# Performance work log

Measured on AMD Instinct MI355X. Metric: run time of the kernel, lower is better.

Reference implementation:

```python
import jax, jax.numpy as jnp
import numpy as np

D_HEAD = 64  # module's self.heads scaling constant


def setup_inputs() -> dict:
    key = jax.random.key(0)
    kq, kk, kv = jax.random.split(key, 3)
    N, HW, C = 4, 4096, 64
    Q = jax.random.normal(kq, (N, HW, C), dtype=jnp.float32)
    K = jax.random.normal(kk, (N, HW, C), dtype=jnp.float32)
    V = jax.random.normal(kv, (N, HW, C), dtype=jnp.float32)
    return {"Q": Q, "K": K, "V": V}


def reference(Q, K, V):
    # logits[n, q, k] = Q[n,q,:] . K[n,k,:] / sqrt(d_head)
    scale = 1.0 / jnp.sqrt(jnp.asarray(D_HEAD, dtype=Q.dtype))
    logits = jnp.einsum("nqc,nkc->nqk", Q, K) * scale  # [N, HW, HW]
    # NOTE: softmax over the QUERY axis (dim=1), non-standard
    attn = jax.nn.softmax(logits, axis=1)
    return jnp.einsum("nqk,nkc->nqc", attn, V)
```

## Files before the change

kernel.cpp:

```cpp
#include <hip/hip_runtime.h>

#define NB 4
#define HWN 4096
#define CD 64
#define NSTRIDE (HWN * CD)

typedef short short8 __attribute__((ext_vector_type(8), may_alias));
typedef float f32x4 __attribute__((ext_vector_type(4), may_alias));

__device__ constexpr float C1 = 0.18033688011112042f;

__device__ __forceinline__ unsigned short f2bf(float f) {
    unsigned u = __builtin_bit_cast(unsigned, f);
    u = (u + 0x7FFFu + ((u >> 16) & 1u)) >> 16;
    return (unsigned short)u;
}

__device__ __forceinline__ float fexp2(float x) {
#if __has_builtin(__builtin_amdgcn_exp2f)
    return __builtin_amdgcn_exp2f(x);
#else
    return exp2f(x);
#endif
}

__device__ __forceinline__ size_t qk_swz(int row, int c) {
    return (size_t)(row >> 4) * 1024 + (c >> 5) * 512 +
           ((((c >> 3) & 3) * 16 + (row & 15)) * 8) + (c & 7);
}

__global__ __launch_bounds__(256) void cvt_qk(const float* __restrict__ Q,
                                              const float* __restrict__ K,
                                              unsigned short* __restrict__ Qs,
                                              unsigned short* __restrict__ Ks) {
    int i = (blockIdx.x * 256 + threadIdx.x) * 4;
    int rg = i >> 6, c = i & 63;
    int n = rg >> 12, r = rg & 4095;
    float4 q = *(const float4*)(Q + i);
    float4 k = *(const float4*)(K + i);
    ushort4 qo, ko;
    qo.x = f2bf(q.x); qo.y = f2bf(q.y); qo.z = f2bf(q.z); qo.w = f2bf(q.w);
    ko.x = f2bf(k.x); ko.y = f2bf(k.y); ko.z = f2bf(k.z); ko.w = f2bf(k.w);
    size_t off = (size_t)n * NSTRIDE + qk_swz(r, c);
    *(ushort4*)(Qs + off) = qo;
    *(ushort4*)(Ks + off) = ko;
}

__global__ __launch_bounds__(256, 4) void lsum_kernel(const unsigned short* __restrict__ Qs,
                                                      const unsigned short* __restrict__ Ks,
                                                      float* __restrict__ l) {
    int tid = threadIdx.x;
    int w = tid >> 6, lane = tid & 63, quad = lane >> 4, m16 = lane & 15;
    int n = blockIdx.y;
    int kbase = blockIdx.x * 128 + w * 32;

    const unsigned short* Kp = Ks + (size_t)n * NSTRIDE + (kbase >> 4) * 1024 + lane * 8;
    short8 ka0 = *(const short8*)(Kp);
    short8 ka1 = *(const short8*)(Kp + 512);
    short8 kb0 = *(const short8*)(Kp + 1024);
    short8 kb1 = *(const short8*)(Kp + 1536);

    const unsigned short* Qp = Qs + (size_t)n * NSTRIDE + blockIdx.z * 32768 + lane * 8;

    float lA[4] = {0.f, 0.f, 0.f, 0.f};
    float lB[4] = {0.f, 0.f, 0.f, 0.f};
#pragma unroll 4
    for (int qc = 0; qc < 32; ++qc) {
        short8 qf0 = *(const short8*)(Qp);
        short8 qf1 = *(const short8*)(Qp + 512);
        f32x4 a = {0.f, 0.f, 0.f, 0.f}, b = {0.f, 0.f, 0.f, 0.f};
        a = __builtin_amdgcn_mfma_f32_16x16x32_bf16(ka0, qf0, a, 0, 0, 0);
        a = __builtin_amdgcn_mfma_f32_16x16x32_bf16(ka1, qf1, a, 0, 0, 0);
        b = __builtin_amdgcn_mfma_f32_16x16x32_bf16(kb0, qf0, b, 0, 0, 0);
        b = __builtin_amdgcn_mfma_f32_16x16x32_bf16(kb1, qf1, b, 0, 0, 0);
#pragma unroll
        for (int r = 0; r < 4; ++r) {
            lA[r] += fexp2(a[r] * C1);
            lB[r] += fexp2(b[r] * C1);
        }
        Qp += 1024;
    }
#pragma unroll
    for (int r = 0; r < 4; ++r)
        for (int d = 1; d < 16; d <<= 1) {
            lA[r] += __shfl_xor(lA[r], d);
            lB[r] += __shfl_xor(lB[r], d);
        }
    if (m16 == 0) {
        float* lp = l + n * HWN + kbase + quad * 4;
#pragma unroll
        for (int r = 0; r < 4; ++r) {
            atomicAdd(lp + r, lA[r]);
            atomicAdd(lp + 16 + r, lB[r]);
        }
    }
}

__global__ __launch_bounds__(256) void prep_v(const float* __restrict__ V,
                                              const float* __restrict__ l,
                                              unsigned short* __restrict__ Vts) {
    __shared__ float rl[64];
    __shared__ float tile[64][65];
    int tid = threadIdx.x, n = blockIdx.y, kbase = blockIdx.x * 64;
    if (tid < 64) rl[tid] = 1.0f / l[n * HWN + kbase + tid];
    __syncthreads();
#pragma unroll
    for (int i = 0; i < 16; ++i) {
        int e = i * 256 + tid;
        int k = e >> 6, c = e & 63;
        tile[c][k] = V[((size_t)(n * HWN + kbase + k)) * CD + c] * rl[k];
    }
    __syncthreads();
#pragma unroll
    for (int i = 0; i < 2; ++i) {
        int s = i * 256 + tid;
        int c = s >> 3, kg = s & 7;
        int kl = kg * 8;
        int kgl = kbase + kl;
        short8 v;
#pragma unroll
        for (int j = 0; j < 8; ++j) v[j] = (short)f2bf(tile[c][kl + j]);
        size_t off = (size_t)n * NSTRIDE + (size_t)(kgl >> 5) * 2048 + (c >> 4) * 512 +
                     ((((kgl >> 3) & 3) * 16 + (c & 15)) * 8);
        *(short8*)(Vts + off) = v;
    }
}

__global__ __launch_bounds__(256, 4) void attn_kernel(const unsigned short* __restrict__ Qs,
                                                      const unsigned short* __restrict__ Ks,
                                                      const unsigned short* __restrict__ Vts,
                                                      float* __restrict__ partial,
                                                      int nseg) {
    __shared__ short plds[4][16][40];
    int tid = threadIdx.x;
    int w = tid >> 6, lane = tid & 63, quad = lane >> 4, m16 = lane & 15;
    int n = blockIdx.y;
    int qbase = blockIdx.x * 64 + w * 16;

    const unsigned short* Qp = Qs + (size_t)n * NSTRIDE + (qbase >> 4) * 1024 + lane * 8;
    short8 qf0 = *(const short8*)(Qp);
    short8 qf1 = *(const short8*)(Qp + 512);

    size_t kofs = (size_t)blockIdx.z * (size_t)nseg * 8 * 2048;
    const unsigned short* Kp = Ks + (size_t)n * NSTRIDE + kofs + lane * 8;
    const unsigned short* Vp = Vts + (size_t)n * NSTRIDE + kofs + lane * 8;

    f32x4 o[4];
#pragma unroll
    for (int ct = 0; ct < 4; ++ct) o[ct] = f32x4{0.f, 0.f, 0.f, 0.f};

    short* pw = &plds[w][0][0];

    for (int seg = 0; seg < nseg; ++seg) {
#pragma unroll
        for (int it = 0; it < 8; ++it) {
            short8 kf00 = *(const short8*)(Kp);
            short8 kf01 = *(const short8*)(Kp + 512);
            short8 kf10 = *(const short8*)(Kp + 1024);
            short8 kf11 = *(const short8*)(Kp + 1536);
            f32x4 s0 = {0.f, 0.f, 0.f, 0.f}, s1 = {0.f, 0.f, 0.f, 0.f};
            s0 = __builtin_amdgcn_mfma_f32_16x16x32_bf16(qf0, kf00, s0, 0, 0, 0);
            s0 = __builtin_amdgcn_mfma_f32_16x16x32_bf16(qf1, kf01, s0, 0, 0, 0);
            s1 = __builtin_amdgcn_mfma_f32_16x16x32_bf16(qf0, kf10, s1, 0, 0, 0);
            s1 = __builtin_amdgcn_mfma_f32_16x16x32_bf16(qf1, kf11, s1, 0, 0, 0);

            short* prow = pw + (quad * 4) * 40 + m16;
#pragma unroll
            for (int r = 0; r < 4; ++r) {
                prow[r * 40]      = (short)f2bf(fexp2(s0[r] * C1));
                prow[r * 40 + 16] = (short)f2bf(fexp2(s1[r] * C1));
            }
            short8 pf = *(const short8*)(pw + m16 * 40 + quad * 8);

#pragma unroll
            for (int ct = 0; ct < 4; ++ct) {
                short8 vf = *(const short8*)(Vp + ct * 512);
                o[ct] = __builtin_amdgcn_mfma_f32_16x16x32_bf16(pf, vf, o[ct], 0, 0, 0);
            }
            Kp += 2048;
            Vp += 2048;
        }
        __syncthreads();
    }

    float* pp = partial + (size_t)blockIdx.z * (NB * HWN * CD) +
                ((size_t)(n * HWN + qbase + quad * 4)) * CD + m16;
#pragma unroll
    for (int ct = 0; ct < 4; ++ct)
#pragma unroll
        for (int r = 0; r < 4; ++r)
            pp[r * CD + ct * 16] = o[ct][r];
}

__global__ __launch_bounds__(256) void reduce_out(const float* __restrict__ p,
                                                  float* __restrict__ out, int ns) {
    int i = (blockIdx.x * 256 + threadIdx.x) * 4;
    f32x4 a = *(const f32x4*)(p + i);
    for (int s = 1; s < ns; ++s)
        a = a + *(const f32x4*)(p + (size_t)s * (NB * HWN * CD) + i);
    *(f32x4*)(out + i) = a;
}

extern "C" void kernel_launch(void* const* d_in, const int* in_sizes, int n_in,
                              void* d_out, int out_size, void* d_ws, size_t ws_size,
                              hipStream_t stream) {
    const float* Q = (const float*)d_in[0];
    const float* K = (const float*)d_in[1];
    const float* V = (const float*)d_in[2];
    float* out = (float*)d_out;

    char* ws = (char*)d_ws;
    unsigned short* Qs  = (unsigned short*)(ws);
    unsigned short* Ks  = (unsigned short*)(ws + (1u << 21));
    unsigned short* Vts = (unsigned short*)(ws + (2u << 21));
    float* l       = (float*)(ws + (3u << 21));
    float* partial = (float*)(ws + (4u << 21));

    size_t base = (size_t)(4u << 21);
    size_t slice = (size_t)NB * HWN * CD * sizeof(float);
    int ns = (ws_size >= base + 4 * slice) ? 4 : 2;
    int nseg = (HWN / ns) / 32 / 8;

    hipMemsetAsync(l, 0, (size_t)NB * HWN * sizeof(float), stream);

    cvt_qk<<<1024, 256, 0, stream>>>(Q, K, Qs, Ks);
    lsum_kernel<<<dim3(32, NB, 8), 256, 0, stream>>>(Qs, Ks, l);
    prep_v<<<dim3(64, NB), 256, 0, stream>>>(V, l, Vts);
    attn_kernel<<<dim3(64, NB, ns), 256, 0, stream>>>(Qs, Ks, Vts, partial, nseg);
    reduce_out<<<1024, 256, 0, stream>>>(partial, out, ns);
}
```

Measured before the change: 133.0 us.

## Software-pipeline attention loop with double-buffered P tile and prefetched K/V

The attention kernel's inner loop is restructured into a software pipeline. It prefetches the next K and V fragments into registers and double-buffers the per-wave P tile in LDS, so the exp/P write for one step overlaps the PV MFMAs of the previous step. The per-segment __syncthreads is removed. The lsum kernel is split across twice as many z-blocks with a register prefetch of Q and an occupancy hint of 8, which raises parallelism and latency hiding. These changes add register pressure and rely on per-wave LDS ordering with no block barrier.

```diff
diff --git a/kernel.cpp b/kernel.cpp
--- a/kernel.cpp
+++ b/kernel.cpp
@@ -46,7 +46,7 @@
     *(ushort4*)(Ks + off) = ko;
 }
 
-__global__ __launch_bounds__(256, 4) void lsum_kernel(const unsigned short* __restrict__ Qs,
+__global__ __launch_bounds__(256, 8) void lsum_kernel(const unsigned short* __restrict__ Qs,
                                                       const unsigned short* __restrict__ Ks,
                                                       float* __restrict__ l) {
     int tid = threadIdx.x;
@@ -60,24 +60,29 @@
     short8 kb0 = *(const short8*)(Kp + 1024);
     short8 kb1 = *(const short8*)(Kp + 1536);
 
-    const unsigned short* Qp = Qs + (size_t)n * NSTRIDE + blockIdx.z * 32768 + lane * 8;
+    const unsigned short* Qp = Qs + (size_t)n * NSTRIDE + blockIdx.z * 16384 + lane * 8;
+
+    short8 qc0 = *(const short8*)(Qp);
+    short8 qc1 = *(const short8*)(Qp + 512);
+    Qp += 1024;
 
     float lA[4] = {0.f, 0.f, 0.f, 0.f};
     float lB[4] = {0.f, 0.f, 0.f, 0.f};
-#pragma unroll 4
-    for (int qc = 0; qc < 32; ++qc) {
-        short8 qf0 = *(const short8*)(Qp);
-        short8 qf1 = *(const short8*)(Qp + 512);
+#pragma unroll 2
+    for (int qc = 0; qc < 16; ++qc) {
+        short8 qn0 = *(const short8*)(Qp);
+        short8 qn1 = *(const short8*)(Qp + 512);
         f32x4 a = {0.f, 0.f, 0.f, 0.f}, b = {0.f, 0.f, 0.f, 0.f};
-        a = __builtin_amdgcn_mfma_f32_16x16x32_bf16(ka0, qf0, a, 0, 0, 0);
-        a = __builtin_amdgcn_mfma_f32_16x16x32_bf16(ka1, qf1, a, 0, 0, 0);
-        b = __builtin_amdgcn_mfma_f32_16x16x32_bf16(kb0, qf0, b, 0, 0, 0);
-        b = __builtin_amdgcn_mfma_f32_16x16x32_bf16(kb1, qf1, b, 0, 0, 0);
+        a = __builtin_amdgcn_mfma_f32_16x16x32_bf16(ka0, qc0, a, 0, 0, 0);
+        a = __builtin_amdgcn_mfma_f32_16x16x32_bf16(ka1, qc1, a, 0, 0, 0);
+        b = __builtin_amdgcn_mfma_f32_16x16x32_bf16(kb0, qc0, b, 0, 0, 0);
+        b = __builtin_amdgcn_mfma_f32_16x16x32_bf16(kb1, qc1, b, 0, 0, 0);
 #pragma unroll
         for (int r = 0; r < 4; ++r) {
             lA[r] += fexp2(a[r] * C1);
             lB[r] += fexp2(b[r] * C1);
         }
+        qc0 = qn0; qc1 = qn1;
         Qp += 1024;
     }
 #pragma unroll
@@ -130,8 +135,8 @@
                                                       const unsigned short* __restrict__ Ks,
                                                       const unsigned short* __restrict__ Vts,
                                                       float* __restrict__ partial,
-                                                      int nseg) {
-    __shared__ short plds[4][16][40];
+                                                      int nit) {
+    __shared__ short plds[4][2][16][40];
     int tid = threadIdx.x;
     int w = tid >> 6, lane = tid & 63, quad = lane >> 4, m16 = lane & 15;
     int n = blockIdx.y;
@@ -141,7 +146,7 @@
     short8 qf0 = *(const short8*)(Qp);
     short8 qf1 = *(const short8*)(Qp + 512);
 
-    size_t kofs = (size_t)blockIdx.z * (size_t)nseg * 8 * 2048;
+    size_t kofs = (size_t)blockIdx.z * (size_t)nit * 2048;
     const unsigned short* Kp = Ks + (size_t)n * NSTRIDE + kofs + lane * 8;
     const unsigned short* Vp = Vts + (size_t)n * NSTRIDE + kofs + lane * 8;
 
@@ -149,38 +154,89 @@
 #pragma unroll
     for (int ct = 0; ct < 4; ++ct) o[ct] = f32x4{0.f, 0.f, 0.f, 0.f};
 
-    short* pw = &plds[w][0][0];
-
-    for (int seg = 0; seg < nseg; ++seg) {
-#pragma unroll
-        for (int it = 0; it < 8; ++it) {
-            short8 kf00 = *(const short8*)(Kp);
-            short8 kf01 = *(const short8*)(Kp + 512);
-            short8 kf10 = *(const short8*)(Kp + 1024);
-            short8 kf11 = *(const short8*)(Kp + 1536);
-            f32x4 s0 = {0.f, 0.f, 0.f, 0.f}, s1 = {0.f, 0.f, 0.f, 0.f};
-            s0 = __builtin_amdgcn_mfma_f32_16x16x32_bf16(qf0, kf00, s0, 0, 0, 0);
-            s0 = __builtin_amdgcn_mfma_f32_16x16x32_bf16(qf1, kf01, s0, 0, 0, 0);
-            s1 = __builtin_amdgcn_mfma_f32_16x16x32_bf16(qf0, kf10, s1, 0, 0, 0);
-            s1 = __builtin_amdgcn_mfma_f32_16x16x32_bf16(qf1, kf11, s1, 0, 0, 0);
-
-            short* prow = pw + (quad * 4) * 40 + m16;
-#pragma unroll
-            for (int r = 0; r < 4; ++r) {
-                prow[r * 40]      = (short)f2bf(fexp2(s0[r] * C1));
-                prow[r * 40 + 16] = (short)f2bf(fexp2(s1[r] * C1));
-            }
-            short8 pf = *(const short8*)(pw + m16 * 40 + quad * 8);
-
-#pragma unroll
-            for (int ct = 0; ct < 4; ++ct) {
-                short8 vf = *(const short8*)(Vp + ct * 512);
-                o[ct] = __builtin_amdgcn_mfma_f32_16x16x32_bf16(pf, vf, o[ct], 0, 0, 0);
-            }
-            Kp += 2048;
-            Vp += 2048;
-        }
-        __syncthreads();
+    short* pw0 = &plds[w][0][0][0];
+    short* pw1 = &plds[w][1][0][0];
+    int wr_off = (quad * 4) * 40 + m16;
+    int rd_off = m16 * 40 + quad * 8;
+
+    short8 kc0, kc1, kc2, kc3, vp0, vp1, vp2, vp3;
+
+    kc0 = *(const short8*)(Kp);
+    kc1 = *(const short8*)(Kp + 512);
+    kc2 = *(const short8*)(Kp + 1024);
+    kc3 = *(const short8*)(Kp + 1536);
+    Kp += 2048;
+    vp0 = *(const short8*)(Vp);
+    vp1 = *(const short8*)(Vp + 512);
+    vp2 = *(const short8*)(Vp + 1024);
+    vp3 = *(const short8*)(Vp + 1536);
+    Vp += 2048;
+    {
+        f32x4 s0 = {0.f, 0.f, 0.f, 0.f}, s1 = {0.f, 0.f, 0.f, 0.f};
+        s0 = __builtin_amdgcn_mfma_f32_16x16x32_bf16(qf0, kc0, s0, 0, 0, 0);
+        s0 = __builtin_amdgcn_mfma_f32_16x16x32_bf16(qf1, kc1, s0, 0, 0, 0);
+        s1 = __builtin_amdgcn_mfma_f32_16x16x32_bf16(qf0, kc2, s1, 0, 0, 0);
+        s1 = __builtin_amdgcn_mfma_f32_16x16x32_bf16(qf1, kc3, s1, 0, 0, 0);
+        short* prow = pw0 + wr_off;
+#pragma unroll
+        for (int r = 0; r < 4; ++r) {
+            prow[r * 40]      = (short)f2bf(fexp2(s0[r] * C1));
+            prow[r * 40 + 16] = (short)f2bf(fexp2(s1[r] * C1));
+        }
+    }
+    kc0 = *(const short8*)(Kp);
+    kc1 = *(const short8*)(Kp + 512);
+    kc2 = *(const short8*)(Kp + 1024);
+    kc3 = *(const short8*)(Kp + 1536);
+    Kp += 2048;
+
+#pragma unroll 2
+    for (int it = 1; it < nit; ++it) {
+        short8 kn0 = *(const short8*)(Kp);
+        short8 kn1 = *(const short8*)(Kp + 512);
+        short8 kn2 = *(const short8*)(Kp + 1024);
+        short8 kn3 = *(const short8*)(Kp + 1536);
+        Kp += 2048;
+        short8 vn0 = *(const short8*)(Vp);
+        short8 vn1 = *(const short8*)(Vp + 512);
+        short8 vn2 = *(const short8*)(Vp + 1024);
+        short8 vn3 = *(const short8*)(Vp + 1536);
+        Vp += 2048;
+
+        f32x4 s0 = {0.f, 0.f, 0.f, 0.f}, s1 = {0.f, 0.f, 0.f, 0.f};
+        s0 = __builtin_amdgcn_mfma_f32_16x16x32_bf16(qf0, kc0, s0, 0, 0, 0);
+        s0 = __builtin_amdgcn_mfma_f32_16x16x32_bf16(qf1, kc1, s0, 0, 0, 0);
+        s1 = __builtin_amdgcn_mfma_f32_16x16x32_bf16(qf0, kc2, s1, 0, 0, 0);
+        s1 = __builtin_amdgcn_mfma_f32_16x16x32_bf16(qf1, kc3, s1, 0, 0, 0);
+
+        short* pr = ((it & 1) ? pw0 : pw1) + rd_off;
+        short8 pf = *(const short8*)pr;
+#pragma unroll
+        for (int ct = 0; ct < 4; ++ct) {
+            short8 vf;
+            switch (ct) { case 0: vf = vp0; break; case 1: vf = vp1; break;
+                          case 2: vf = vp2; break; default: vf = vp3; }
+            o[ct] = __builtin_amdgcn_mfma_f32_16x16x32_bf16(pf, vf, o[ct], 0, 0, 0);
+        }
+
+        short* prow = ((it & 1) ? pw1 : pw0) + wr_off;
+#pragma unroll
+        for (int r = 0; r < 4; ++r) {
+            prow[r * 40]      = (short)f2bf(fexp2(s0[r] * C1));
+            prow[r * 40 + 16] = (short)f2bf(fexp2(s1[r] * C1));
+        }
+
+        kc0 = kn0; kc1 = kn1; kc2 = kn2; kc3 = kn3;
+        vp0 = vn0; vp1 = vn1; vp2 = vn2; vp3 = vn3;
+    }
+
+    {
+        short* pr = ((nit & 1) ? pw0 : pw1) + rd_off;
+        short8 pf = *(const short8*)pr;
+        o[0] = __builtin_amdgcn_mfma_f32_16x16x32_bf16(pf, vp0, o[0], 0, 0, 0);
+        o[1] = __builtin_amdgcn_mfma_f32_16x16x32_bf16(pf, vp1, o[1], 0, 0, 0);
+        o[2] = __builtin_amdgcn_mfma_f32_16x16x32_bf16(pf, vp2, o[2], 0, 0, 0);
+        o[3] = __builtin_amdgcn_mfma_f32_16x16x32_bf16(pf, vp3, o[3], 0, 0, 0);
     }
 
     float* pp = partial + (size_t)blockIdx.z * (NB * HWN * CD) +
@@ -219,13 +275,13 @@
     size_t base = (size_t)(4u << 21);
     size_t slice = (size_t)NB * HWN * CD * sizeof(float);
     int ns = (ws_size >= base + 4 * slice) ? 4 : 2;
-    int nseg = (HWN / ns) / 32 / 8;
+    int nit = HWN / ns / 32;
 
     hipMemsetAsync(l, 0, (size_t)NB * HWN * sizeof(float), stream);
 
     cvt_qk<<<1024, 256, 0, stream>>>(Q, K, Qs, Ks);
-    lsum_kernel<<<dim3(32, NB, 8), 256, 0, stream>>>(Qs, Ks, l);
+    lsum_kernel<<<dim3(32, NB, 16), 256, 0, stream>>>(Qs, Ks, l);
     prep_v<<<dim3(64, NB), 256, 0, stream>>>(V, l, Vts);
-    attn_kernel<<<dim3(64, NB, ns), 256, 0, stream>>>(Qs, Ks, Vts, partial, nseg);
+    attn_kernel<<<dim3(64, NB, ns), 256, 0, stream>>>(Qs, Ks, Vts, partial, nit);
     reduce_out<<<1024, 256, 0, stream>>>(partial, out, ns);
 }
```

Result: faster. 124.3 us (-6.5%).

## Stage K/V and Q tiles through LDS with async double-buffered loads

Applied to the files above, without the earlier changes.

The attention kernel now copies K and V tiles into double-buffered shared memory using global_load_lds. Each wave handles 32 queries instead of 16, so each K/V fragment is reused twice. The PV matmul is software-pipelined one iteration behind the QK exp stage, and the key-axis split grows to 8 segments when the workspace allows. The lsum kernel also stages Q through LDS, raises its occupancy target and uses twice as many z-blocks. The aim is to cut redundant global loads and hide load latency, at the cost of more LDS, extra barriers per iteration and larger partial buffers to reduce.

```diff
diff --git a/kernel.cpp b/kernel.cpp
--- a/kernel.cpp
+++ b/kernel.cpp
@@ -22,6 +22,12 @@
 #else
     return exp2f(x);
 #endif
+}
+
+__device__ __forceinline__ void gload_lds16(const unsigned short* g, unsigned short* lds) {
+    __builtin_amdgcn_global_load_lds(
+        (const __attribute__((address_space(1))) unsigned int*)g,
+        (__attribute__((address_space(3))) unsigned int*)lds, 16, 0, 0);
 }
 
 __device__ __forceinline__ size_t qk_swz(int row, int c) {
@@ -46,9 +52,10 @@
     *(ushort4*)(Ks + off) = ko;
 }
 
-__global__ __launch_bounds__(256, 4) void lsum_kernel(const unsigned short* __restrict__ Qs,
+__global__ __launch_bounds__(256, 8) void lsum_kernel(const unsigned short* __restrict__ Qs,
                                                       const unsigned short* __restrict__ Ks,
                                                       float* __restrict__ l) {
+    __shared__ unsigned short qstage[2][1024];
     int tid = threadIdx.x;
     int w = tid >> 6, lane = tid & 63, quad = lane >> 4, m16 = lane & 15;
     int n = blockIdx.y;
@@ -60,14 +67,19 @@
     short8 kb0 = *(const short8*)(Kp + 1024);
     short8 kb1 = *(const short8*)(Kp + 1536);
 
-    const unsigned short* Qp = Qs + (size_t)n * NSTRIDE + blockIdx.z * 32768 + lane * 8;
+    const unsigned short* Qsrc = Qs + (size_t)n * NSTRIDE + blockIdx.z * 16384;
+
+    if (w < 2) gload_lds16(Qsrc + w * 512 + lane * 8, &qstage[0][w * 512]);
 
     float lA[4] = {0.f, 0.f, 0.f, 0.f};
     float lB[4] = {0.f, 0.f, 0.f, 0.f};
-#pragma unroll 4
-    for (int qc = 0; qc < 32; ++qc) {
-        short8 qf0 = *(const short8*)(Qp);
-        short8 qf1 = *(const short8*)(Qp + 512);
+    for (int it = 0; it < 16; ++it) {
+        __syncthreads();
+        if (it + 1 < 16 && w < 2)
+            gload_lds16(Qsrc + (it + 1) * 1024 + w * 512 + lane * 8,
+                        &qstage[(it + 1) & 1][w * 512]);
+        short8 qf0 = *(const short8*)&qstage[it & 1][lane * 8];
+        short8 qf1 = *(const short8*)&qstage[it & 1][512 + lane * 8];
         f32x4 a = {0.f, 0.f, 0.f, 0.f}, b = {0.f, 0.f, 0.f, 0.f};
         a = __builtin_amdgcn_mfma_f32_16x16x32_bf16(ka0, qf0, a, 0, 0, 0);
         a = __builtin_amdgcn_mfma_f32_16x16x32_bf16(ka1, qf1, a, 0, 0, 0);
@@ -78,7 +90,6 @@
             lA[r] += fexp2(a[r] * C1);
             lB[r] += fexp2(b[r] * C1);
         }
-        Qp += 1024;
     }
 #pragma unroll
     for (int r = 0; r < 4; ++r)
@@ -130,57 +141,107 @@
                                                       const unsigned short* __restrict__ Ks,
                                                       const unsigned short* __restrict__ Vts,
                                                       float* __restrict__ partial,
-                                                      int nseg) {
-    __shared__ short plds[4][16][40];
+                                                      int nit) {
+    __shared__ unsigned short stage[2][4096];
+    __shared__ short plds[4][2][2][16][40];
     int tid = threadIdx.x;
     int w = tid >> 6, lane = tid & 63, quad = lane >> 4, m16 = lane & 15;
     int n = blockIdx.y;
-    int qbase = blockIdx.x * 64 + w * 16;
+    int qbase = blockIdx.x * 128 + w * 32;
 
     const unsigned short* Qp = Qs + (size_t)n * NSTRIDE + (qbase >> 4) * 1024 + lane * 8;
-    short8 qf0 = *(const short8*)(Qp);
-    short8 qf1 = *(const short8*)(Qp + 512);
-
-    size_t kofs = (size_t)blockIdx.z * (size_t)nseg * 8 * 2048;
-    const unsigned short* Kp = Ks + (size_t)n * NSTRIDE + kofs + lane * 8;
-    const unsigned short* Vp = Vts + (size_t)n * NSTRIDE + kofs + lane * 8;
-
-    f32x4 o[4];
-#pragma unroll
-    for (int ct = 0; ct < 4; ++ct) o[ct] = f32x4{0.f, 0.f, 0.f, 0.f};
-
-    short* pw = &plds[w][0][0];
-
-    for (int seg = 0; seg < nseg; ++seg) {
-#pragma unroll
-        for (int it = 0; it < 8; ++it) {
-            short8 kf00 = *(const short8*)(Kp);
-            short8 kf01 = *(const short8*)(Kp + 512);
-            short8 kf10 = *(const short8*)(Kp + 1024);
-            short8 kf11 = *(const short8*)(Kp + 1536);
-            f32x4 s0 = {0.f, 0.f, 0.f, 0.f}, s1 = {0.f, 0.f, 0.f, 0.f};
-            s0 = __builtin_amdgcn_mfma_f32_16x16x32_bf16(qf0, kf00, s0, 0, 0, 0);
-            s0 = __builtin_amdgcn_mfma_f32_16x16x32_bf16(qf1, kf01, s0, 0, 0, 0);
-            s1 = __builtin_amdgcn_mfma_f32_16x16x32_bf16(qf0, kf10, s1, 0, 0, 0);
-            s1 = __builtin_amdgcn_mfma_f32_16x16x32_bf16(qf1, kf11, s1, 0, 0, 0);
-
-            short* prow = pw + (quad * 4) * 40 + m16;
+    short8 qa0 = *(const short8*)(Qp);
+    short8 qa1 = *(const short8*)(Qp + 512);
+    short8 qb0 = *(const short8*)(Qp + 1024);
+    short8 qb1 = *(const short8*)(Qp + 1536);
+
+    size_t kofs = (size_t)blockIdx.z * (size_t)nit * 2048;
+    const unsigned short* Ksrc = Ks + (size_t)n * NSTRIDE + kofs;
+    const unsigned short* Vsrc = Vts + (size_t)n * NSTRIDE + kofs;
+    const unsigned short* dsrc0 = (w < 2) ? (Ksrc + w * 1024) : (Vsrc + (w - 2) * 1024);
+
+    f32x4 oA[4], oB[4];
+#pragma unroll
+    for (int ct = 0; ct < 4; ++ct) { oA[ct] = f32x4{0.f, 0.f, 0.f, 0.f}; oB[ct] = oA[ct]; }
+
+    int wr = quad * 4 * 40 + m16;
+    int rd = m16 * 40 + quad * 8;
+
+    short8 vp0, vp1, vp2, vp3;
+
+    gload_lds16(dsrc0 + lane * 8, &stage[0][w * 1024]);
+    gload_lds16(dsrc0 + 512 + lane * 8, &stage[0][w * 1024 + 512]);
+
+    for (int it = 0; it < nit; ++it) {
+        __syncthreads();
+        if (it + 1 < nit) {
+            const unsigned short* ds = dsrc0 + (it + 1) * 2048;
+            unsigned short* dd = &stage[(it + 1) & 1][w * 1024];
+            gload_lds16(ds + lane * 8, dd);
+            gload_lds16(ds + 512 + lane * 8, dd + 512);
+        }
+        const unsigned short* kb = &stage[it & 1][0];
+        const unsigned short* vb = &stage[it & 1][2048];
+
+        short8 kf00 = *(const short8*)(kb + lane * 8);
+        short8 kf01 = *(const short8*)(kb + 512 + lane * 8);
+        short8 kf10 = *(const short8*)(kb + 1024 + lane * 8);
+        short8 kf11 = *(const short8*)(kb + 1536 + lane * 8);
+        f32x4 sA0 = {0.f, 0.f, 0.f, 0.f}, sA1 = sA0, sB0 = sA0, sB1 = sA0;
+        sA0 = __builtin_amdgcn_mfma_f32_16x16x32_bf16(qa0, kf00, sA0, 0, 0, 0);
+        sA0 = __builtin_amdgcn_mfma_f32_16x16x32_bf16(qa1, kf01, sA0, 0, 0, 0);
+        sA1 = __builtin_amdgcn_mfma_f32_16x16x32_bf16(qa0, kf10, sA1, 0, 0, 0);
+        sA1 = __builtin_amdgcn_mfma_f32_16x16x32_bf16(qa1, kf11, sA1, 0, 0, 0);
+        sB0 = __builtin_amdgcn_mfma_f32_16x16x32_bf16(qb0, kf00, sB0, 0, 0, 0);
+        sB0 = __builtin_amdgcn_mfma_f32_16x16x32_bf16(qb1, kf01, sB0, 0, 0, 0);
+        sB1 = __builtin_amdgcn_mfma_f32_16x16x32_bf16(qb0, kf10, sB1, 0, 0, 0);
+        sB1 = __builtin_amdgcn_mfma_f32_16x16x32_bf16(qb1, kf11, sB1, 0, 0, 0);
+
+        if (it > 0) {
+            int pb = (it - 1) & 1;
+            short8 pfA = *(const short8*)(&plds[w][pb][0][0][0] + rd);
+            short8 pfB = *(const short8*)(&plds[w][pb][1][0][0] + rd);
+            oA[0] = __builtin_amdgcn_mfma_f32_16x16x32_bf16(pfA, vp0, oA[0], 0, 0, 0);
+            oA[1] = __builtin_amdgcn_mfma_f32_16x16x32_bf16(pfA, vp1, oA[1], 0, 0, 0);
+            oA[2] = __builtin_amdgcn_mfma_f32_16x16x32_bf16(pfA, vp2, oA[2], 0, 0, 0);
+            oA[3] = __builtin_amdgcn_mfma_f32_16x16x32_bf16(pfA, vp3, oA[3], 0, 0, 0);
+            oB[0] = __builtin_amdgcn_mfma_f32_16x16x32_bf16(pfB, vp0, oB[0], 0, 0, 0);
+            oB[1] = __builtin_amdgcn_mfma_f32_16x16x32_bf16(pfB, vp1, oB[1], 0, 0, 0);
+            oB[2] = __builtin_amdgcn_mfma_f32_16x16x32_bf16(pfB, vp2, oB[2], 0, 0, 0);
+            oB[3] = __builtin_amdgcn_mfma_f32_16x16x32_bf16(pfB, vp3, oB[3], 0, 0, 0);
+        }
+
+        {
+            int pb = it & 1;
+            short* pA = &plds[w][pb][0][0][0] + wr;
+            short* pB = &plds[w][pb][1][0][0] + wr;
 #pragma unroll
             for (int r = 0; r < 4; ++r) {
-                prow[r * 40]      = (short)f2bf(fexp2(s0[r] * C1));
-                prow[r * 40 + 16] = (short)f2bf(fexp2(s1[r] * C1));
+                pA[r * 40]      = (short)f2bf(fexp2(sA0[r] * C1));
+                pA[r * 40 + 16] = (short)f2bf(fexp2(sA1[r] * C1));
+                pB[r * 40]      = (short)f2bf(fexp2(sB0[r] * C1));
+                pB[r * 40 + 16] = (short)f2bf(fexp2(sB1[r] * C1));
             }
-            short8 pf = *(const short8*)(pw + m16 * 40 + quad * 8);
-
-#pragma unroll
-            for (int ct = 0; ct < 4; ++ct) {
-                short8 vf = *(const short8*)(Vp + ct * 512);
-                o[ct] = __builtin_amdgcn_mfma_f32_16x16x32_bf16(pf, vf, o[ct], 0, 0, 0);
-            }
-            Kp += 2048;
-            Vp += 2048;
-        }
-        __syncthreads();
+        }
+
+        vp0 = *(const short8*)(vb + lane * 8);
+        vp1 = *(const short8*)(vb + 512 + lane * 8);
+        vp2 = *(const short8*)(vb + 1024 + lane * 8);
+        vp3 = *(const short8*)(vb + 1536 + lane * 8);
+    }
+
+    {
+        int pb = (nit - 1) & 1;
+        short8 pfA = *(const short8*)(&plds[w][pb][0][0][0] + rd);
+        short8 pfB = *(const short8*)(&plds[w][pb][1][0][0] + rd);
+        oA[0] = __builtin_amdgcn_mfma_f32_16x16x32_bf16(pfA, vp0, oA[0], 0, 0, 0);
+        oA[1] = __builtin_amdgcn_mfma_f32_16x16x32_bf16(pfA, vp1, oA[1], 0, 0, 0);
+        oA[2] = __builtin_amdgcn_mfma_f32_16x16x32_bf16(pfA, vp2, oA[2], 0, 0, 0);
+        oA[3] = __builtin_amdgcn_mfma_f32_16x16x32_bf16(pfA, vp3, oA[3], 0, 0, 0);
+        oB[0] = __builtin_amdgcn_mfma_f32_16x16x32_bf16(pfB, vp0, oB[0], 0, 0, 0);
+        oB[1] = __builtin_amdgcn_mfma_f32_16x16x32_bf16(pfB, vp1, oB[1], 0, 0, 0);
+        oB[2] = __builtin_amdgcn_mfma_f32_16x16x32_bf16(pfB, vp2, oB[2], 0, 0, 0);
+        oB[3] = __builtin_amdgcn_mfma_f32_16x16x32_bf16(pfB, vp3, oB[3], 0, 0, 0);
     }
 
     float* pp = partial + (size_t)blockIdx.z * (NB * HWN * CD) +
@@ -188,8 +249,10 @@
 #pragma unroll
     for (int ct = 0; ct < 4; ++ct)
 #pragma unroll
-        for (int r = 0; r < 4; ++r)
-            pp[r * CD + ct * 16] = o[ct][r];
+        for (int r = 0; r < 4; ++r) {
+            pp[r * CD + ct * 16] = oA[ct][r];
+            pp[(16 + r) * CD + ct * 16] = oB[ct][r];
+        }
 }
 
 __global__ __launch_bounds__(256) void reduce_out(const float* __restrict__ p,
@@ -218,14 +281,15 @@
 
     size_t base = (size_t)(4u << 21);
     size_t slice = (size_t)NB * HWN * CD * sizeof(float);
-    int ns = (ws_size >= base + 4 * slice) ? 4 : 2;
-    int nseg = (HWN / ns) / 32 / 8;
+    int ns = (ws_size >= base + 8 * slice) ? 8
+           : (ws_size >= base + 4 * slice) ? 4 : 2;
+    int nit = HWN / ns / 32;
 
     hipMemsetAsync(l, 0, (size_t)NB * HWN * sizeof(float), stream);
 
     cvt_qk<<<1024, 256, 0, stream>>>(Q, K, Qs, Ks);
-    lsum_kernel<<<dim3(32, NB, 8), 256, 0, stream>>>(Qs, Ks, l);
+    lsum_kernel<<<dim3(32, NB, 16), 256, 0, stream>>>(Qs, Ks, l);
     prep_v<<<dim3(64, NB), 256, 0, stream>>>(V, l, Vts);
-    attn_kernel<<<dim3(64, NB, ns), 256, 0, stream>>>(Qs, Ks, Vts, partial, nseg);
+    attn_kernel<<<dim3(32, NB, ns), 256, 0, stream>>>(Qs, Ks, Vts, partial, nit);
     reduce_out<<<1024, 256, 0, stream>>>(partial, out, ns);
 }
```

New measurement: 312.8 us. +135.2%, slower.

## Keep attention probabilities in registers via transposed MFMA, fold scale into Q

Applied to the files above, without the earlier changes.

The attention kernel now computes transposed score tiles (K as the A operand), so the exp'd probabilities already sit in the MFMA B-operand layout. Two 16x16x16 bf16 MFMAs per V tile consume them directly, which removes the LDS round-trip and the per-segment barrier. The V layout is permuted to match, the softmax scale is folded into Q during conversion, and output stores become vectorised. The lsum kernel handles 64 keys per wave with prefetched Q fragments and a reshaped grid. The costs are extra rounding from pre-scaling Q in bf16 and more registers.

```diff
diff --git a/kernel.cpp b/kernel.cpp
--- a/kernel.cpp
+++ b/kernel.cpp
@@ -6,6 +6,7 @@
 #define NSTRIDE (HWN * CD)
 
 typedef short short8 __attribute__((ext_vector_type(8), may_alias));
+typedef short short4v __attribute__((ext_vector_type(4), may_alias));
 typedef float f32x4 __attribute__((ext_vector_type(4), may_alias));
 
 __device__ constexpr float C1 = 0.18033688011112042f;
@@ -39,52 +40,73 @@
     float4 q = *(const float4*)(Q + i);
     float4 k = *(const float4*)(K + i);
     ushort4 qo, ko;
-    qo.x = f2bf(q.x); qo.y = f2bf(q.y); qo.z = f2bf(q.z); qo.w = f2bf(q.w);
+    qo.x = f2bf(q.x * C1); qo.y = f2bf(q.y * C1);
+    qo.z = f2bf(q.z * C1); qo.w = f2bf(q.w * C1);
     ko.x = f2bf(k.x); ko.y = f2bf(k.y); ko.z = f2bf(k.z); ko.w = f2bf(k.w);
     size_t off = (size_t)n * NSTRIDE + qk_swz(r, c);
     *(ushort4*)(Qs + off) = qo;
     *(ushort4*)(Ks + off) = ko;
 }
 
-__global__ __launch_bounds__(256, 4) void lsum_kernel(const unsigned short* __restrict__ Qs,
-                                                      const unsigned short* __restrict__ Ks,
-                                                      float* __restrict__ l) {
+__global__ __attribute__((amdgpu_flat_work_group_size(256, 256), amdgpu_waves_per_eu(2, 4)))
+void lsum_kernel(const unsigned short* __restrict__ Qs,
+                 const unsigned short* __restrict__ Ks,
+                 float* __restrict__ l) {
     int tid = threadIdx.x;
     int w = tid >> 6, lane = tid & 63, quad = lane >> 4, m16 = lane & 15;
     int n = blockIdx.y;
-    int kbase = blockIdx.x * 128 + w * 32;
+    int kbase = blockIdx.x * 256 + w * 64;
 
     const unsigned short* Kp = Ks + (size_t)n * NSTRIDE + (kbase >> 4) * 1024 + lane * 8;
     short8 ka0 = *(const short8*)(Kp);
     short8 ka1 = *(const short8*)(Kp + 512);
     short8 kb0 = *(const short8*)(Kp + 1024);
     short8 kb1 = *(const short8*)(Kp + 1536);
-
-    const unsigned short* Qp = Qs + (size_t)n * NSTRIDE + blockIdx.z * 32768 + lane * 8;
+    short8 kc0 = *(const short8*)(Kp + 2048);
+    short8 kc1 = *(const short8*)(Kp + 2560);
+    short8 kd0 = *(const short8*)(Kp + 3072);
+    short8 kd1 = *(const short8*)(Kp + 3584);
+
+    const unsigned short* Qp = Qs + (size_t)n * NSTRIDE + blockIdx.z * 16384 + lane * 8;
+
+    short8 qc0 = *(const short8*)(Qp);
+    short8 qc1 = *(const short8*)(Qp + 512);
+    Qp += 1024;
 
     float lA[4] = {0.f, 0.f, 0.f, 0.f};
     float lB[4] = {0.f, 0.f, 0.f, 0.f};
-#pragma unroll 4
-    for (int qc = 0; qc < 32; ++qc) {
-        short8 qf0 = *(const short8*)(Qp);
-        short8 qf1 = *(const short8*)(Qp + 512);
-        f32x4 a = {0.f, 0.f, 0.f, 0.f}, b = {0.f, 0.f, 0.f, 0.f};
-        a = __builtin_amdgcn_mfma_f32_16x16x32_bf16(ka0, qf0, a, 0, 0, 0);
-        a = __builtin_amdgcn_mfma_f32_16x16x32_bf16(ka1, qf1, a, 0, 0, 0);
-        b = __builtin_amdgcn_mfma_f32_16x16x32_bf16(kb0, qf0, b, 0, 0, 0);
-        b = __builtin_amdgcn_mfma_f32_16x16x32_bf16(kb1, qf1, b, 0, 0, 0);
+    float lC[4] = {0.f, 0.f, 0.f, 0.f};
+    float lD[4] = {0.f, 0.f, 0.f, 0.f};
+#pragma unroll 2
+    for (int qc = 0; qc < 16; ++qc) {
+        short8 qn0 = *(const short8*)(Qp);
+        short8 qn1 = *(const short8*)(Qp + 512);
+        f32x4 a = {0.f, 0.f, 0.f, 0.f}, b = a, c = a, d = a;
+        a = __builtin_amdgcn_mfma_f32_16x16x32_bf16(ka0, qc0, a, 0, 0, 0);
+        a = __builtin_amdgcn_mfma_f32_16x16x32_bf16(ka1, qc1, a, 0, 0, 0);
+        b = __builtin_amdgcn_mfma_f32_16x16x32_bf16(kb0, qc0, b, 0, 0, 0);
+        b = __builtin_amdgcn_mfma_f32_16x16x32_bf16(kb1, qc1, b, 0, 0, 0);
+        c = __builtin_amdgcn_mfma_f32_16x16x32_bf16(kc0, qc0, c, 0, 0, 0);
+        c = __builtin_amdgcn_mfma_f32_16x16x32_bf16(kc1, qc1, c, 0, 0, 0);
+        d = __builtin_amdgcn_mfma_f32_16x16x32_bf16(kd0, qc0, d, 0, 0, 0);
+        d = __builtin_amdgcn_mfma_f32_16x16x32_bf16(kd1, qc1, d, 0, 0, 0);
 #pragma unroll
         for (int r = 0; r < 4; ++r) {
-            lA[r] += fexp2(a[r] * C1);
-            lB[r] += fexp2(b[r] * C1);
-        }
+            lA[r] += fexp2(a[r]);
+            lB[r] += fexp2(b[r]);
+            lC[r] += fexp2(c[r]);
+            lD[r] += fexp2(d[r]);
+        }
+        qc0 = qn0; qc1 = qn1;
         Qp += 1024;
     }
 #pragma unroll
     for (int r = 0; r < 4; ++r)
-        for (int d = 1; d < 16; d <<= 1) {
-            lA[r] += __shfl_xor(lA[r], d);
-            lB[r] += __shfl_xor(lB[r], d);
+        for (int d1 = 1; d1 < 16; d1 <<= 1) {
+            lA[r] += __shfl_xor(lA[r], d1);
+            lB[r] += __shfl_xor(lB[r], d1);
+            lC[r] += __shfl_xor(lC[r], d1);
+            lD[r] += __shfl_xor(lD[r], d1);
         }
     if (m16 == 0) {
         float* lp = l + n * HWN + kbase + quad * 4;
@@ -92,6 +114,8 @@
         for (int r = 0; r < 4; ++r) {
             atomicAdd(lp + r, lA[r]);
             atomicAdd(lp + 16 + r, lB[r]);
+            atomicAdd(lp + 32 + r, lC[r]);
+            atomicAdd(lp + 48 + r, lD[r]);
         }
     }
 }
@@ -114,24 +138,30 @@
 #pragma unroll
     for (int i = 0; i < 2; ++i) {
         int s = i * 256 + tid;
-        int c = s >> 3, kg = s & 7;
-        int kl = kg * 8;
-        int kgl = kbase + kl;
+        int kb32 = s >> 8;
+        int ct = (s >> 6) & 3;
+        int ll = s & 63;
+        int cc = ct * 16 + (ll & 15);
+        int kq = ((ll >> 4) & 3) * 4;
+        int k0 = kb32 * 32 + kq;
         short8 v;
 #pragma unroll
-        for (int j = 0; j < 8; ++j) v[j] = (short)f2bf(tile[c][kl + j]);
-        size_t off = (size_t)n * NSTRIDE + (size_t)(kgl >> 5) * 2048 + (c >> 4) * 512 +
-                     ((((kgl >> 3) & 3) * 16 + (c & 15)) * 8);
+        for (int j = 0; j < 4; ++j) {
+            v[j]     = (short)f2bf(tile[cc][k0 + j]);
+            v[4 + j] = (short)f2bf(tile[cc][k0 + 16 + j]);
+        }
+        size_t off = (size_t)n * NSTRIDE + (size_t)((kbase >> 5) + kb32) * 2048 +
+                     ct * 512 + ll * 8;
         *(short8*)(Vts + off) = v;
     }
 }
 
-__global__ __launch_bounds__(256, 4) void attn_kernel(const unsigned short* __restrict__ Qs,
-                                                      const unsigned short* __restrict__ Ks,
-                                                      const unsigned short* __restrict__ Vts,
-                                                      float* __restrict__ partial,
-                                                      int nseg) {
-    __shared__ short plds[4][16][40];
+__global__ __attribute__((amdgpu_flat_work_group_size(256, 256), amdgpu_waves_per_eu(2, 4)))
+void attn_kernel(const unsigned short* __restrict__ Qs,
+                 const unsigned short* __restrict__ Ks,
+                 const unsigned short* __restrict__ Vts,
+                 float* __restrict__ partial,
+                 int nit) {
     int tid = threadIdx.x;
     int w = tid >> 6, lane = tid & 63, quad = lane >> 4, m16 = lane & 15;
     int n = blockIdx.y;
@@ -141,7 +171,7 @@
     short8 qf0 = *(const short8*)(Qp);
     short8 qf1 = *(const short8*)(Qp + 512);
 
-    size_t kofs = (size_t)blockIdx.z * (size_t)nseg * 8 * 2048;
+    size_t kofs = (size_t)blockIdx.z * (size_t)nit * 2048;
     const unsigned short* Kp = Ks + (size_t)n * NSTRIDE + kofs + lane * 8;
     const unsigned short* Vp = Vts + (size_t)n * NSTRIDE + kofs + lane * 8;
 
@@ -149,47 +179,42 @@
 #pragma unroll
     for (int ct = 0; ct < 4; ++ct) o[ct] = f32x4{0.f, 0.f, 0.f, 0.f};
 
-    short* pw = &plds[w][0][0];
-
-    for (int seg = 0; seg < nseg; ++seg) {
-#pragma unroll
-        for (int it = 0; it < 8; ++it) {
-            short8 kf00 = *(const short8*)(Kp);
-            short8 kf01 = *(const short8*)(Kp + 512);
-            short8 kf10 = *(const short8*)(Kp + 1024);
-            short8 kf11 = *(const short8*)(Kp + 1536);
-            f32x4 s0 = {0.f, 0.f, 0.f, 0.f}, s1 = {0.f, 0.f, 0.f, 0.f};
-            s0 = __builtin_amdgcn_mfma_f32_16x16x32_bf16(qf0, kf00, s0, 0, 0, 0);
-            s0 = __builtin_amdgcn_mfma_f32_16x16x32_bf16(qf1, kf01, s0, 0, 0, 0);
-            s1 = __builtin_amdgcn_mfma_f32_16x16x32_bf16(qf0, kf10, s1, 0, 0, 0);
-            s1 = __builtin_amdgcn_mfma_f32_16x16x32_bf16(qf1, kf11, s1, 0, 0, 0);
-
-            short* prow = pw + (quad * 4) * 40 + m16;
-#pragma unroll
-            for (int r = 0; r < 4; ++r) {
-                prow[r * 40]      = (short)f2bf(fexp2(s0[r] * C1));
-                prow[r * 40 + 16] = (short)f2bf(fexp2(s1[r] * C1));
-            }
-            short8 pf = *(const short8*)(pw + m16 * 40 + quad * 8);
-
-#pragma unroll
-            for (int ct = 0; ct < 4; ++ct) {
-                short8 vf = *(const short8*)(Vp + ct * 512);
-                o[ct] = __builtin_amdgcn_mfma_f32_16x16x32_bf16(pf, vf, o[ct], 0, 0, 0);
-            }
-            Kp += 2048;
-            Vp += 2048;
-        }
-        __syncthreads();
+#pragma unroll 2
+    for (int it = 0; it < nit; ++it) {
+        short8 kf00 = *(const short8*)(Kp);
+        short8 kf01 = *(const short8*)(Kp + 512);
+        short8 kf10 = *(const short8*)(Kp + 1024);
+        short8 kf11 = *(const short8*)(Kp + 1536);
+        f32x4 sA = {0.f, 0.f, 0.f, 0.f}, sB = sA;
+        sA = __builtin_amdgcn_mfma_f32_16x16x32_bf16(kf00, qf0, sA, 0, 0, 0);
+        sA = __builtin_amdgcn_mfma_f32_16x16x32_bf16(kf01, qf1, sA, 0, 0, 0);
+        sB = __builtin_amdgcn_mfma_f32_16x16x32_bf16(kf10, qf0, sB, 0, 0, 0);
+        sB = __builtin_amdgcn_mfma_f32_16x16x32_bf16(kf11, qf1, sB, 0, 0, 0);
+
+        short4v pA, pB;
+#pragma unroll
+        for (int r = 0; r < 4; ++r) {
+            pA[r] = (short)f2bf(fexp2(sA[r]));
+            pB[r] = (short)f2bf(fexp2(sB[r]));
+        }
+
+#pragma unroll
+        for (int ct = 0; ct < 4; ++ct) {
+            short8 vf = *(const short8*)(Vp + ct * 512);
+            short4v vlo = __builtin_shufflevector(vf, vf, 0, 1, 2, 3);
+            short4v vhi = __builtin_shufflevector(vf, vf, 4, 5, 6, 7);
+            o[ct] = __builtin_amdgcn_mfma_f32_16x16x16bf16_1k(vlo, pA, o[ct], 0, 0, 0);
+            o[ct] = __builtin_amdgcn_mfma_f32_16x16x16bf16_1k(vhi, pB, o[ct], 0, 0, 0);
+        }
+        Kp += 2048;
+        Vp += 2048;
     }
 
     float* pp = partial + (size_t)blockIdx.z * (NB * HWN * CD) +
-                ((size_t)(n * HWN + qbase + quad * 4)) * CD + m16;
+                ((size_t)(n * HWN + qbase + m16)) * CD + quad * 4;
 #pragma unroll
     for (int ct = 0; ct < 4; ++ct)
-#pragma unroll
-        for (int r = 0; r < 4; ++r)
-            pp[r * CD + ct * 16] = o[ct][r];
+        *(f32x4*)(pp + ct * 16) = o[ct];
 }
 
 __global__ __launch_bounds__(256) void reduce_out(const float* __restrict__ p,
@@ -219,13 +244,13 @@
     size_t base = (size_t)(4u << 21);
     size_t slice = (size_t)NB * HWN * CD * sizeof(float);
     int ns = (ws_size >= base + 4 * slice) ? 4 : 2;
-    int nseg = (HWN / ns) / 32 / 8;
-
-    hipMemsetAsync(l, 0, (size_t)NB * HWN * sizeof(float), stream);
+    int nit = HWN / ns / 32;
+
+    (void)hipMemsetAsync(l, 0, (size_t)NB * HWN * sizeof(float), stream);
 
     cvt_qk<<<1024, 256, 0, stream>>>(Q, K, Qs, Ks);
-    lsum_kernel<<<dim3(32, NB, 8), 256, 0, stream>>>(Qs, Ks, l);
+    lsum_kernel<<<dim3(16, NB, 16), 256, 0, stream>>>(Qs, Ks, l);
     prep_v<<<dim3(64, NB), 256, 0, stream>>>(V, l, Vts);
-    attn_kernel<<<dim3(64, NB, ns), 256, 0, stream>>>(Qs, Ks, Vts, partial, nseg);
+    attn_kernel<<<dim3(64, NB, ns), 256, 0, stream>>>(Qs, Ks, Vts, partial, nit);
     reduce_out<<<1024, 256, 0, stream>>>(partial, out, ns);
 }
```

Measured after the change: 123.0 us. 1.08x faster.
